# Kernel tuning notes

Measured on AMD Instinct MI355X. Metric: run time of the kernel, lower is better.

The kernel has to match this reference:

```python
import jax, jax.numpy as jnp
import numpy as np

NEG_INF = -1e9
LRELU_SLOPE = 0.2


def setup_inputs() -> dict:
    N, F_IN, F_OUT = 8192, 256, 128
    key = jax.random.key(0)
    k_adj, k_x, k_w, k_phi = jax.random.split(key, 4)
    adj = (jax.random.uniform(k_adj, (N, N)) < 0.01).astype(jnp.float32)
    x = jax.random.normal(k_x, (N, F_IN), dtype=jnp.float32)
    stdv_w = 1.0 / np.sqrt(F_OUT)
    weight = jax.random.uniform(k_w, (F_IN, F_OUT), minval=-stdv_w, maxval=stdv_w, dtype=jnp.float32)
    bias = jnp.zeros((F_OUT,), dtype=jnp.float32)
    phi = jax.random.uniform(k_phi, (2 * F_OUT, 1), minval=-1.0, maxval=1.0, dtype=jnp.float32)
    return {"adj": adj, "input": x, "weight": weight, "bias": bias, "phi": phi}


def reference(adj, input, weight, bias, phi):
    # x_prime: [N, F_OUT]
    x_prime = input @ weight + bias
    N = adj.shape[0]
    F_out = x_prime.shape[1]
    # S[i, j] = cat(x_i, x_j) @ phi = x_i @ phi[:F] + x_j @ phi[F:]
    # (identical math to the repeat+cat formulation, without the O(N^2*2F) tensor)
    phi_src = phi[:F_out, 0]  # [F_OUT]
    phi_dst = phi[F_out:, 0]  # [F_OUT]
    s_src = x_prime @ phi_src  # [N]
    s_dst = x_prime @ phi_dst  # [N]
    S = s_src[:, None] + s_dst[None, :]  # [N, N]
    S = jnp.where(S >= 0, S, LRELU_SLOPE * S)  # leaky_relu(0.2)
    mask = (adj + jnp.eye(N, dtype=adj.dtype)) > 0
    S_masked = jnp.where(mask, S, NEG_INF)
    attention = jax.nn.softmax(S_masked, axis=1)  # row-wise
    h = attention @ x_prime  # [N, F_OUT]
    return h
```

## Files before the change

kernel.cpp:

```cpp
#include <hip/hip_runtime.h>

#define Nn    8192
#define FIN   256
#define FOUTc 128
#define MAXN  512

__global__ __launch_bounds__(256) void k_xprime(const float* __restrict__ x,
                                                const float* __restrict__ w,
                                                const float* __restrict__ bias,
                                                const float* __restrict__ phi,
                                                float* __restrict__ xp,
                                                float* __restrict__ s_src,
                                                float* __restrict__ s_dst)
{
    __shared__ float Wl[64 * 128];
    __shared__ float Xl[32][68];
    __shared__ float Ssum[4][16], Dsum[4][16];

    const int tid = threadIdx.x;
    const int c = tid & 127, g = tid >> 7;
    const int wv_ = tid >> 6, lane = tid & 63;
    const int row0 = blockIdx.x * 32;

    float acc[16];
    const float bv = bias[c];
#pragma unroll
    for (int r = 0; r < 16; r++) acc[r] = bv;

    for (int ko = 0; ko < FIN; ko += 64) {
#pragma unroll
        for (int t = 0; t < 8; t++) {
            const int idx = t * 1024 + tid * 4;
            *(float4*)&Wl[idx] = *(const float4*)&w[(size_t)ko * FOUTc + idx];
        }
#pragma unroll
        for (int t = 0; t < 2; t++) {
            const int idx = t * 1024 + tid * 4;
            const int r = idx >> 6, k = idx & 63;
            const float4 v = *(const float4*)&x[(size_t)(row0 + r) * FIN + ko + k];
            Xl[r][k] = v.x; Xl[r][k + 1] = v.y; Xl[r][k + 2] = v.z; Xl[r][k + 3] = v.w;
        }
        __syncthreads();
        for (int k = 0; k < 64; k++) {
            const float wvv = Wl[k * FOUTc + c];
#pragma unroll
            for (int r = 0; r < 16; r++)
                acc[r] = fmaf(Xl[g * 16 + r][k], wvv, acc[r]);
        }
        __syncthreads();
    }

#pragma unroll
    for (int r = 0; r < 16; r++)
        xp[(size_t)(row0 + g * 16 + r) * FOUTc + c] = acc[r];

    const float phs = phi[c], phd = phi[FOUTc + c];
#pragma unroll
    for (int r = 0; r < 16; r++) {
        float ps = acc[r] * phs;
        float pd = acc[r] * phd;
#pragma unroll
        for (int off = 32; off > 0; off >>= 1) {
            ps += __shfl_down(ps, off, 64);
            pd += __shfl_down(pd, off, 64);
        }
        if (lane == 0) { Ssum[wv_][r] = ps; Dsum[wv_][r] = pd; }
    }
    __syncthreads();
    if (tid < 32) {
        const int g2 = tid >> 4, r = tid & 15;
        const int row = row0 + g2 * 16 + r;
        s_src[row] = Ssum[2 * g2][r] + Ssum[2 * g2 + 1][r];
        s_dst[row] = Dsum[2 * g2][r] + Dsum[2 * g2 + 1][r];
    }
}

__global__ __launch_bounds__(256) void k_scan(const float* __restrict__ adj,
                                              int* __restrict__ g_cnt,
                                              int* __restrict__ g_nbr)
{
    __shared__ int nbr[MAXN];
    __shared__ int cnt;
    const int tid = threadIdx.x;
    const int i = blockIdx.x;
    if (tid == 0) cnt = 0;
    __syncthreads();

    const float4* arow4 = (const float4*)(adj + (size_t)i * Nn);
    float4 buf[8];
#pragma unroll
    for (int t = 0; t < 8; t++) buf[t] = arow4[t * 256 + tid];

#pragma unroll
    for (int t = 0; t < 8; t++) {
        const int j0 = (t * 256 + tid) * 4;
        const float av[4] = {buf[t].x, buf[t].y, buf[t].z, buf[t].w};
#pragma unroll
        for (int p = 0; p < 4; p++) {
            const int j = j0 + p;
            if (av[p] != 0.f || j == i) {
                const int pos = atomicAdd(&cnt, 1);
                if (pos < MAXN) nbr[pos] = j;
            }
        }
    }
    __syncthreads();
    const int L = (cnt < MAXN) ? cnt : MAXN;
    if (tid == 0) g_cnt[i] = L;
    for (int n = tid; n < L; n += 256)
        g_nbr[(size_t)i * MAXN + n] = nbr[n];
}

__global__ __launch_bounds__(256) void k_soft(const int* __restrict__ g_cnt,
                                              const int* __restrict__ g_nbr,
                                              const float* __restrict__ s_src,
                                              const float* __restrict__ s_dst,
                                              const float* __restrict__ xp,
                                              float* __restrict__ out)
{
    __shared__ int   js[MAXN];
    __shared__ float wts[MAXN];
    __shared__ float ph[2][FOUTc];
    __shared__ float red[4];

    const int tid = threadIdx.x;
    const int i = blockIdx.x;
    const int L = g_cnt[i];

    float lmax = -1e30f;
    for (int n = tid; n < L; n += 256) {
        const int j = g_nbr[(size_t)i * MAXN + n];
        js[n] = j;
        const float sd = s_dst[j];
        wts[n] = sd;
        lmax = fmaxf(lmax, sd);
    }
#pragma unroll
    for (int off = 32; off > 0; off >>= 1) lmax = fmaxf(lmax, __shfl_down(lmax, off, 64));
    if ((tid & 63) == 0) red[tid >> 6] = lmax;
    __syncthreads();
    const float maxd = fmaxf(fmaxf(red[0], red[1]), fmaxf(red[2], red[3]));
    const float ssi = s_src[i];
    const float Sm  = ssi + maxd;
    const float m_i = (Sm >= 0.f) ? Sm : 0.2f * Sm;

    float lsum = 0.f;
    for (int n = tid; n < L; n += 256) {
        float S = ssi + wts[n];
        S = (S >= 0.f) ? S : 0.2f * S;
        const float wv = __expf(S - m_i);
        wts[n] = wv;
        lsum += wv;
    }
#pragma unroll
    for (int off = 32; off > 0; off >>= 1) lsum += __shfl_down(lsum, off, 64);
    __syncthreads();
    if ((tid & 63) == 0) red[tid >> 6] = lsum;
    __syncthreads();
    const float inv = 1.f / ((red[0] + red[1]) + (red[2] + red[3]));

    const int c = tid & 127, half = tid >> 7;
    float h = 0.f;
    for (int n = half; n < L; n += 2)
        h = fmaf(wts[n], xp[(size_t)js[n] * FOUTc + c], h);
    ph[half][c] = h;
    __syncthreads();
    if (tid < FOUTc)
        out[(size_t)i * FOUTc + tid] = (ph[0][tid] + ph[1][tid]) * inv;
}

extern "C" void kernel_launch(void* const* d_in, const int* in_sizes, int n_in,
                              void* d_out, int out_size, void* d_ws, size_t ws_size,
                              hipStream_t stream)
{
    (void)out_size; (void)ws_size;
    const float* adj  = (const float*)d_in[0];
    const float* x    = (const float*)d_in[1];
    const float* w    = (const float*)d_in[2];
    const float* bias = (const float*)d_in[3];
    const float* phi  = (const float*)d_in[4];
    for (int i = 0; i < n_in; i++) {
        switch (in_sizes[i]) {
            case Nn * Nn:     adj  = (const float*)d_in[i]; break;
            case Nn * FIN:    x    = (const float*)d_in[i]; break;
            case FIN * FOUTc: w    = (const float*)d_in[i]; break;
            case FOUTc:       bias = (const float*)d_in[i]; break;
            case 2 * FOUTc:   phi  = (const float*)d_in[i]; break;
        }
    }
    float* out = (float*)d_out;

    char* ws = (char*)d_ws;
    float* xp    = (float*)ws;
    float* s_src = (float*)(ws + (size_t)Nn * FOUTc * 4);
    float* s_dst = s_src + Nn;
    int*   g_cnt = (int*)(s_dst + Nn);
    int*   g_nbr = g_cnt + Nn;

    hipLaunchKernelGGL(k_xprime, dim3(Nn / 32), dim3(256), 0, stream,
                       x, w, bias, phi, xp, s_src, s_dst);
    hipLaunchKernelGGL(k_scan,   dim3(Nn),      dim3(256), 0, stream, adj, g_cnt, g_nbr);
    hipLaunchKernelGGL(k_soft,   dim3(Nn),      dim3(256), 0, stream,
                       g_cnt, g_nbr, s_src, s_dst, xp, out);
}
```

Baseline: 454.1 us.

## Fuse adjacency scan with softmax aggregation and compact nonzero quads via ballot

```diff
diff --git a/kernel.cpp b/kernel.cpp
--- a/kernel.cpp
+++ b/kernel.cpp
@@ -4,6 +4,7 @@
 #define FIN   256
 #define FOUTc 128
 #define MAXN  512
+#define QCAP  128
 
 __global__ __launch_bounds__(256) void k_xprime(const float* __restrict__ x,
                                                 const float* __restrict__ w,
@@ -75,29 +76,64 @@
     }
 }
 
-__global__ __launch_bounds__(256) void k_scan(const float* __restrict__ adj,
-                                              int* __restrict__ g_cnt,
-                                              int* __restrict__ g_nbr)
+__global__ __launch_bounds__(256) void k_gat(const float* __restrict__ adj,
+                                             const float* __restrict__ s_src,
+                                             const float* __restrict__ s_dst,
+                                             const float* __restrict__ xp,
+                                             float* __restrict__ out)
 {
-    __shared__ int nbr[MAXN];
-    __shared__ int cnt;
+    __shared__ int   qseg[4][QCAP];
+    __shared__ int   ql[4 * QCAP];
+    __shared__ int   qn[4], qoff[5];
+    __shared__ int   nbr[MAXN];
+    __shared__ float wts[MAXN];
+    __shared__ float ph[2][FOUTc];
+    __shared__ float red[4];
+    __shared__ int   cnt;
+
     const int tid = threadIdx.x;
+    const int lane = tid & 63, wv = tid >> 6;
     const int i = blockIdx.x;
     if (tid == 0) cnt = 0;
-    __syncthreads();
 
     const float4* arow4 = (const float4*)(adj + (size_t)i * Nn);
     float4 buf[8];
 #pragma unroll
-    for (int t = 0; t < 8; t++) buf[t] = arow4[t * 256 + tid];
-
-#pragma unroll
-    for (int t = 0; t < 8; t++) {
-        const int j0 = (t * 256 + tid) * 4;
-        const float av[4] = {buf[t].x, buf[t].y, buf[t].z, buf[t].w};
+    for (int q = 0; q < 8; q++) buf[q] = arow4[wv * 512 + q * 64 + lane];
+
+    const int dq = i >> 2;
+    int qc = 0;
+#pragma unroll
+    for (int q = 0; q < 8; q++) {
+        const int quad = wv * 512 + q * 64 + lane;
+        const uint4 u = *(const uint4*)&buf[q];
+        const bool any = ((u.x | u.y | u.z | u.w) != 0u) || (quad == dq);
+        const unsigned long long m = __ballot(any);
+        if (any) {
+            const int pos = qc + (int)__popcll(m & ((1ull << lane) - 1ull));
+            if (pos < QCAP) qseg[wv][pos] = quad;
+        }
+        qc += (int)__popcll(m);
+    }
+    if (lane == 0) qn[wv] = (qc < QCAP) ? qc : QCAP;
+    __syncthreads();
+    if (tid == 0) {
+        qoff[0] = 0;
+        for (int w = 0; w < 4; w++) qoff[w + 1] = qoff[w] + qn[w];
+    }
+    __syncthreads();
+    for (int n = lane; n < qn[wv]; n += 64) ql[qoff[wv] + n] = qseg[wv][n];
+    __syncthreads();
+    const int Q = qoff[4];
+
+    const float* arow = adj + (size_t)i * Nn;
+    for (int n = tid; n < Q; n += 256) {
+        const int quad = ql[n];
+        const float4 v = *(const float4*)(arow + (size_t)quad * 4);
+        const float av[4] = {v.x, v.y, v.z, v.w};
 #pragma unroll
         for (int p = 0; p < 4; p++) {
-            const int j = j0 + p;
+            const int j = quad * 4 + p;
             if (av[p] != 0.f || j == i) {
                 const int pos = atomicAdd(&cnt, 1);
                 if (pos < MAXN) nbr[pos] = j;
@@ -106,38 +142,16 @@
     }
     __syncthreads();
     const int L = (cnt < MAXN) ? cnt : MAXN;
-    if (tid == 0) g_cnt[i] = L;
-    for (int n = tid; n < L; n += 256)
-        g_nbr[(size_t)i * MAXN + n] = nbr[n];
-}
-
-__global__ __launch_bounds__(256) void k_soft(const int* __restrict__ g_cnt,
-                                              const int* __restrict__ g_nbr,
-                                              const float* __restrict__ s_src,
-                                              const float* __restrict__ s_dst,
-                                              const float* __restrict__ xp,
-                                              float* __restrict__ out)
-{
-    __shared__ int   js[MAXN];
-    __shared__ float wts[MAXN];
-    __shared__ float ph[2][FOUTc];
-    __shared__ float red[4];
-
-    const int tid = threadIdx.x;
-    const int i = blockIdx.x;
-    const int L = g_cnt[i];
 
     float lmax = -1e30f;
     for (int n = tid; n < L; n += 256) {
-        const int j = g_nbr[(size_t)i * MAXN + n];
-        js[n] = j;
-        const float sd = s_dst[j];
+        const float sd = s_dst[nbr[n]];
         wts[n] = sd;
         lmax = fmaxf(lmax, sd);
     }
 #pragma unroll
     for (int off = 32; off > 0; off >>= 1) lmax = fmaxf(lmax, __shfl_down(lmax, off, 64));
-    if ((tid & 63) == 0) red[tid >> 6] = lmax;
+    if (lane == 0) red[wv] = lmax;
     __syncthreads();
     const float maxd = fmaxf(fmaxf(red[0], red[1]), fmaxf(red[2], red[3]));
     const float ssi = s_src[i];
@@ -148,21 +162,21 @@
     for (int n = tid; n < L; n += 256) {
         float S = ssi + wts[n];
         S = (S >= 0.f) ? S : 0.2f * S;
-        const float wv = __expf(S - m_i);
-        wts[n] = wv;
-        lsum += wv;
+        const float wvv = __expf(S - m_i);
+        wts[n] = wvv;
+        lsum += wvv;
     }
 #pragma unroll
     for (int off = 32; off > 0; off >>= 1) lsum += __shfl_down(lsum, off, 64);
     __syncthreads();
-    if ((tid & 63) == 0) red[tid >> 6] = lsum;
+    if (lane == 0) red[wv] = lsum;
     __syncthreads();
     const float inv = 1.f / ((red[0] + red[1]) + (red[2] + red[3]));
 
     const int c = tid & 127, half = tid >> 7;
     float h = 0.f;
     for (int n = half; n < L; n += 2)
-        h = fmaf(wts[n], xp[(size_t)js[n] * FOUTc + c], h);
+        h = fmaf(wts[n], xp[(size_t)nbr[n] * FOUTc + c], h);
     ph[half][c] = h;
     __syncthreads();
     if (tid < FOUTc)
@@ -194,12 +208,9 @@
     float* xp    = (float*)ws;
     float* s_src = (float*)(ws + (size_t)Nn * FOUTc * 4);
     float* s_dst = s_src + Nn;
-    int*   g_cnt = (int*)(s_dst + Nn);
-    int*   g_nbr = g_cnt + Nn;
 
     hipLaunchKernelGGL(k_xprime, dim3(Nn / 32), dim3(256), 0, stream,
                        x, w, bias, phi, xp, s_src, s_dst);
-    hipLaunchKernelGGL(k_scan,   dim3(Nn),      dim3(256), 0, stream, adj, g_cnt, g_nbr);
-    hipLaunchKernelGGL(k_soft,   dim3(Nn),      dim3(256), 0, stream,
-                       g_cnt, g_nbr, s_src, s_dst, xp, out);
+    hipLaunchKernelGGL(k_gat,    dim3(Nn),      dim3(256), 0, stream,
+                       adj, s_src, s_dst, xp, out);
 }
```

After: 428.7 us. 5.6% less time.

## Grid-stride adjacency scan with wave ballot compaction and vectorized aggregation

Applied to the files above, without the earlier changes.

```diff
diff --git a/kernel.cpp b/kernel.cpp
--- a/kernel.cpp
+++ b/kernel.cpp
@@ -4,6 +4,8 @@
 #define FIN   256
 #define FOUTc 128
 #define MAXN  512
+#define NQ    (Nn * Nn / 4)
+#define SCANT (1024 * 256)
 
 __global__ __launch_bounds__(256) void k_xprime(const float* __restrict__ x,
                                                 const float* __restrict__ w,
@@ -75,57 +77,61 @@
     }
 }
 
-__global__ __launch_bounds__(256) void k_scan(const float* __restrict__ adj,
-                                              int* __restrict__ g_cnt,
-                                              int* __restrict__ g_nbr)
-{
-    __shared__ int nbr[MAXN];
-    __shared__ int cnt;
-    const int tid = threadIdx.x;
-    const int i = blockIdx.x;
-    if (tid == 0) cnt = 0;
-    __syncthreads();
-
-    const float4* arow4 = (const float4*)(adj + (size_t)i * Nn);
-    float4 buf[8];
-#pragma unroll
-    for (int t = 0; t < 8; t++) buf[t] = arow4[t * 256 + tid];
-
-#pragma unroll
-    for (int t = 0; t < 8; t++) {
-        const int j0 = (t * 256 + tid) * 4;
-        const float av[4] = {buf[t].x, buf[t].y, buf[t].z, buf[t].w};
-#pragma unroll
-        for (int p = 0; p < 4; p++) {
-            const int j = j0 + p;
-            if (av[p] != 0.f || j == i) {
-                const int pos = atomicAdd(&cnt, 1);
-                if (pos < MAXN) nbr[pos] = j;
-            }
-        }
-    }
-    __syncthreads();
-    const int L = (cnt < MAXN) ? cnt : MAXN;
-    if (tid == 0) g_cnt[i] = L;
-    for (int n = tid; n < L; n += 256)
-        g_nbr[(size_t)i * MAXN + n] = nbr[n];
-}
-
-__global__ __launch_bounds__(256) void k_soft(const int* __restrict__ g_cnt,
-                                              const int* __restrict__ g_nbr,
-                                              const float* __restrict__ s_src,
-                                              const float* __restrict__ s_dst,
-                                              const float* __restrict__ xp,
-                                              float* __restrict__ out)
+__global__ __launch_bounds__(256) void k_scan2(const uint4* __restrict__ adjq,
+                                               int* __restrict__ g_cnt,
+                                               int* __restrict__ g_nbr)
+{
+    const int lane = threadIdx.x & 63;
+    const int gtid = blockIdx.x * 256 + threadIdx.x;
+    const unsigned long long lt = (1ull << lane) - 1ull;
+#pragma unroll 2
+    for (int it = 0; it < NQ / SCANT; ++it) {
+        const int q = gtid + it * SCANT;
+        const uint4 u = adjq[q];
+        const int r = q >> 11;
+        const int colq = q & 2047;
+        bool b0 = (u.x != 0u), b1 = (u.y != 0u), b2 = (u.z != 0u), b3 = (u.w != 0u);
+        if (colq == (r >> 2)) {
+            const int comp = r & 3;
+            b0 |= (comp == 0); b1 |= (comp == 1); b2 |= (comp == 2); b3 |= (comp == 3);
+        }
+        const unsigned long long m0 = __ballot(b0);
+        const unsigned long long m1 = __ballot(b1);
+        const unsigned long long m2 = __ballot(b2);
+        const unsigned long long m3 = __ballot(b3);
+        const int t0 = __popcll(m0), t1 = __popcll(m1), t2 = __popcll(m2), t3 = __popcll(m3);
+        const int total = t0 + t1 + t2 + t3;
+        if (total) {
+            int base = 0;
+            if (lane == 0) base = atomicAdd(&g_cnt[r], total);
+            base = __shfl(base, 0, 64);
+            int* dst = g_nbr + (size_t)r * MAXN;
+            const int c4 = colq * 4;
+            if (b0) { const int i0 = base + __popcll(m0 & lt);                 if (i0 < MAXN) dst[i0] = c4; }
+            if (b1) { const int i1 = base + t0 + __popcll(m1 & lt);            if (i1 < MAXN) dst[i1] = c4 + 1; }
+            if (b2) { const int i2 = base + t0 + t1 + __popcll(m2 & lt);       if (i2 < MAXN) dst[i2] = c4 + 2; }
+            if (b3) { const int i3 = base + t0 + t1 + t2 + __popcll(m3 & lt);  if (i3 < MAXN) dst[i3] = c4 + 3; }
+        }
+    }
+}
+
+__global__ __launch_bounds__(256) void k_soft2(const int* __restrict__ g_cnt,
+                                               const int* __restrict__ g_nbr,
+                                               const float* __restrict__ s_src,
+                                               const float* __restrict__ s_dst,
+                                               const float* __restrict__ xp,
+                                               float* __restrict__ out)
 {
     __shared__ int   js[MAXN];
     __shared__ float wts[MAXN];
-    __shared__ float ph[2][FOUTc];
+    __shared__ float ph[8][132];
     __shared__ float red[4];
 
     const int tid = threadIdx.x;
+    const int lane = tid & 63, wv = tid >> 6;
     const int i = blockIdx.x;
-    const int L = g_cnt[i];
+    const int cntv = g_cnt[i];
+    const int L = (cntv < MAXN) ? cntv : MAXN;
 
     float lmax = -1e30f;
     for (int n = tid; n < L; n += 256) {
@@ -137,7 +143,7 @@
     }
 #pragma unroll
     for (int off = 32; off > 0; off >>= 1) lmax = fmaxf(lmax, __shfl_down(lmax, off, 64));
-    if ((tid & 63) == 0) red[tid >> 6] = lmax;
+    if (lane == 0) red[wv] = lmax;
     __syncthreads();
     const float maxd = fmaxf(fmaxf(red[0], red[1]), fmaxf(red[2], red[3]));
     const float ssi = s_src[i];
@@ -148,25 +154,34 @@
     for (int n = tid; n < L; n += 256) {
         float S = ssi + wts[n];
         S = (S >= 0.f) ? S : 0.2f * S;
-        const float wv = __expf(S - m_i);
-        wts[n] = wv;
-        lsum += wv;
+        const float wvv = __expf(S - m_i);
+        wts[n] = wvv;
+        lsum += wvv;
     }
 #pragma unroll
     for (int off = 32; off > 0; off >>= 1) lsum += __shfl_down(lsum, off, 64);
     __syncthreads();
-    if ((tid & 63) == 0) red[tid >> 6] = lsum;
+    if (lane == 0) red[wv] = lsum;
     __syncthreads();
     const float inv = 1.f / ((red[0] + red[1]) + (red[2] + red[3]));
 
-    const int c = tid & 127, half = tid >> 7;
-    float h = 0.f;
-    for (int n = half; n < L; n += 2)
-        h = fmaf(wts[n], xp[(size_t)js[n] * FOUTc + c], h);
-    ph[half][c] = h;
-    __syncthreads();
-    if (tid < FOUTc)
-        out[(size_t)i * FOUTc + tid] = (ph[0][tid] + ph[1][tid]) * inv;
+    const int g = tid >> 5, t = tid & 31;
+    float4 h = make_float4(0.f, 0.f, 0.f, 0.f);
+    for (int n = g; n < L; n += 8) {
+        const float wvv = wts[n];
+        const float4 xv = *(const float4*)&xp[(size_t)js[n] * FOUTc + t * 4];
+        h.x = fmaf(wvv, xv.x, h.x);
+        h.y = fmaf(wvv, xv.y, h.y);
+        h.z = fmaf(wvv, xv.z, h.z);
+        h.w = fmaf(wvv, xv.w, h.w);
+    }
+    *(float4*)&ph[g][t * 4] = h;
+    __syncthreads();
+    if (tid < FOUTc) {
+        const float s = ((ph[0][tid] + ph[1][tid]) + (ph[2][tid] + ph[3][tid]))
+                      + ((ph[4][tid] + ph[5][tid]) + (ph[6][tid] + ph[7][tid]));
+        out[(size_t)i * FOUTc + tid] = s * inv;
+    }
 }
 
 extern "C" void kernel_launch(void* const* d_in, const int* in_sizes, int n_in,
@@ -197,9 +212,11 @@
     int*   g_cnt = (int*)(s_dst + Nn);
     int*   g_nbr = g_cnt + Nn;
 
+    hipMemsetAsync(g_cnt, 0, Nn * sizeof(int), stream);
     hipLaunchKernelGGL(k_xprime, dim3(Nn / 32), dim3(256), 0, stream,
                        x, w, bias, phi, xp, s_src, s_dst);
-    hipLaunchKernelGGL(k_scan,   dim3(Nn),      dim3(256), 0, stream, adj, g_cnt, g_nbr);
-    hipLaunchKernelGGL(k_soft,   dim3(Nn),      dim3(256), 0, stream,
+    hipLaunchKernelGGL(k_scan2,  dim3(SCANT / 256), dim3(256), 0, stream,
+                       (const uint4*)adj, g_cnt, g_nbr);
+    hipLaunchKernelGGL(k_soft2,  dim3(Nn), dim3(256), 0, stream,
                        g_cnt, g_nbr, s_src, s_dst, xp, out);
 }
```

Measured after the change: 452.5 us. Within noise of the previous version (-0.4%).
